# Kernel tuning notes

Hardware: AMD Instinct MI355X
Metric: run time of the kernel (lower is better)

## Reference

```python
import jax, jax.numpy as jnp
import numpy as np

B, T, C = 16, 512, 1024
D, K, W = 4096, 128, 8


def _scatter_topk(a, k, use_values):
    """Top-k along last axis; return dense array with top-k values (or 1.0) scattered, zeros elsewhere."""
    shp = a.shape
    a2 = a.reshape(-1, shp[-1])
    vals, idx = jax.lax.top_k(a2, k)
    rows = jnp.arange(a2.shape[0])[:, None]
    src = vals if use_values else jnp.ones_like(vals)
    return jnp.zeros_like(a2).at[rows, idx].set(src).reshape(shp)


def _window_topk(x, k, window_size):
    # x: (B, T, D)
    b, t, d = x.shape
    stride = max(1, window_size // 2)
    if stride >= t:
        num_windows, pad, t_pad = 1, 0, t
    else:
        num_windows = (t - window_size) // stride + 1
        required = (num_windows - 1) * stride + window_size
        pad = max(0, required - t)
        t_pad = t + pad
    if pad > 0:
        x = jnp.pad(x, ((0, 0), (0, pad), (0, 0)))
    starts = jnp.arange(num_windows) * stride                      # (NW,)
    tidx = starts[:, None] + jnp.arange(window_size)               # (NW, W)
    x_windows = x[:, tidx, :]                                      # (B, NW, W, D)
    window_sums = x_windows.sum(axis=2)                            # (B, NW, D)
    mask_windows = _scatter_topk(window_sums, k, use_values=False)  # (B, NW, D)
    votes = (x_windows * mask_windows[:, :, None, :]).reshape(b, num_windows * window_size, d)
    feature_votes = jnp.zeros((b, t_pad, d), x.dtype).at[:, tidx.reshape(-1)].add(votes)
    mask_combined = _scatter_topk(feature_votes, k, use_values=False)  # (B, Tp, D)
    x_sparse = x * mask_combined
    return x_sparse[:, :t - 0, :] if pad > 0 else x_sparse


def setup_inputs() -> dict:
    key = jax.random.key(0)
    ks = jax.random.split(key, 4)
    x_ssl = jax.random.normal(ks[0], (B, T, C), jnp.float32)
    W_dec = jax.random.normal(ks[1], (C, D), jnp.float32)
    W_dec = W_dec / jnp.linalg.norm(W_dec, axis=0, keepdims=True)
    W_enc = W_dec.T                                                # tied init, as in module
    W1 = jax.random.normal(ks[2], (256, D), jnp.float32) * (1.0 / np.sqrt(D))
    W2 = jax.random.normal(ks[3], (2, 256), jnp.float32) * (1.0 / np.sqrt(256))
    return dict(
        x_ssl=x_ssl, W_enc=W_enc, b_enc=jnp.zeros((D,), jnp.float32),
        W_dec=W_dec, b_dec=jnp.zeros((C,), jnp.float32),
        ln_g=jnp.ones((D,), jnp.float32), ln_b=jnp.zeros((D,), jnp.float32),
        W1=W1, b1=jnp.zeros((256,), jnp.float32),
        W2=W2, b2=jnp.zeros((2,), jnp.float32),
    )


def reference(x_ssl, W_enc, b_enc, W_dec, b_dec, ln_g, ln_b, W1, b1, W2, b2):
    b, t, c = x_ssl.shape
    x_flat = x_ssl.reshape(b * t, c)
    # SAE encode with window top-k (window_size=8 > 1 path)
    pre = jnp.einsum('nc,dc->nd', x_flat - b_dec, W_enc) + b_enc
    post_relu = jax.nn.relu(pre).reshape(b, t, -1)                 # (B, T, D)
    encoded = _window_topk(post_relu, K, W)                        # (B, T, D)
    encoded_flat = encoded.reshape(b * t, -1)
    # SAE decode + reconstruction loss
    x_recon = jnp.einsum('nd,cd->nc', encoded_flat, W_dec) + b_dec
    sae_loss = jnp.mean((x_recon - x_flat) ** 2)
    # classifier on pooled sparse features (dropout is inference no-op)
    pooled = encoded.mean(axis=1)                                  # (B, D) == AdaptiveAvgPool1d(1)
    mu = pooled.mean(axis=-1, keepdims=True)
    var = pooled.var(axis=-1, keepdims=True)
    ln = (pooled - mu) / jnp.sqrt(var + 1e-5) * ln_g + ln_b
    h = jax.nn.relu(ln @ W1.T + b1)
    logits = h @ W2.T + b2
    log_probs = jax.nn.log_softmax(logits, axis=-1)
    return log_probs, sae_loss
```

## Files before the change

### kernel.cpp

```cpp
#include <hip/hip_runtime.h>

#define BB   16
#define TT   512
#define CC   1024
#define DD   4096
#define NN   (BB*TT)
#define NWIN 127
#define KTOP 128

typedef __attribute__((ext_vector_type(8))) short short8;
typedef __attribute__((ext_vector_type(8))) unsigned short ushort8;
typedef _Float16 half8 __attribute__((ext_vector_type(8)));
typedef __attribute__((ext_vector_type(4))) float f32x4;

__device__ __forceinline__ unsigned short f2bf(float f) {
    unsigned u = __float_as_uint(f);
    unsigned r = (u + 0x7fffu + ((u >> 16) & 1u)) >> 16;
    return (unsigned short)r;
}
__device__ __forceinline__ unsigned short f2h(float f) {
    union { _Float16 h; unsigned short u; } c;
    c.h = (_Float16)f;
    return c.u;
}
__device__ __forceinline__ float h2f(unsigned short u) {
    union { unsigned short u; _Float16 h; } c;
    c.u = u;
    return (float)c.h;
}
__device__ __forceinline__ unsigned tokey(float f) {
    unsigned u = __float_as_uint(f);
    return (u & 0x80000000u) ? ~u : (u | 0x80000000u);
}
__device__ __forceinline__ void async_lds16(const void* g, void* l) {
    __builtin_amdgcn_global_load_lds((const __attribute__((address_space(1))) void*)g,
                                     (__attribute__((address_space(3))) void*)l, 16, 0, 0);
}

__device__ __forceinline__ unsigned wave_prefix_incl(unsigned v) {
    int lane = threadIdx.x & 63;
#pragma unroll
    for (int off = 1; off < 64; off <<= 1) {
        unsigned n = __shfl_up(v, off, 64);
        if (lane >= off) v += n;
    }
    return v;
}
__device__ __forceinline__ unsigned wave_suffix_incl(unsigned v) {
    int lane = threadIdx.x & 63;
#pragma unroll
    for (int off = 1; off < 64; off <<= 1) {
        unsigned n = __shfl_down(v, off, 64);
        if (lane + off < 64) v += n;
    }
    return v;
}

__device__ __forceinline__ unsigned select_top128(const unsigned* keys,
                                                  unsigned* hist, unsigned* shx) {
    const int tid = threadIdx.x, wid = tid >> 6, lane = tid & 63;
    const unsigned ZKEY = 0x80000000u;
    unsigned cpos = 0, cz = 0;
#pragma unroll
    for (int i = 0; i < 16; ++i) {
        cpos += (keys[i] > ZKEY);
        cz   += (keys[i] == ZKEY);
    }
    unsigned ppos = wave_prefix_incl(cpos);
    unsigned pz   = wave_prefix_incl(cz);
    if (lane == 63) { shx[wid] = ppos; shx[4 + wid] = pz; }
    __syncthreads();
    unsigned nz = shx[0] + shx[1] + shx[2] + shx[3];
    unsigned selbits = 0u;
    if (nz <= KTOP) {
        unsigned need = KTOP - nz;
        unsigned zr = pz - cz;
        if (wid > 0) zr += shx[4];
        if (wid > 1) zr += shx[5];
        if (wid > 2) zr += shx[6];
#pragma unroll
        for (int i = 0; i < 16; ++i) {
            bool sel = (keys[i] > ZKEY) || (keys[i] == ZKEY && zr < need);
            if (keys[i] == ZKEY) ++zr;
            selbits |= (sel ? 1u : 0u) << i;
        }
        return selbits;
    }
    unsigned k2[16];
#pragma unroll
    for (int i = 0; i < 16; ++i) k2[i] = (keys[i] > ZKEY) ? keys[i] : 0u;
    unsigned prefix = 0u, pmask = 0u, Kr = KTOP;
    for (int shift = 24; shift >= 0; shift -= 8) {
        hist[tid] = 0u; hist[256 + tid] = 0u; hist[512 + tid] = 0u; hist[768 + tid] = 0u;
        __syncthreads();
        unsigned* h = hist + (wid << 8);
#pragma unroll
        for (int i = 0; i < 16; ++i)
            if (k2[i] && (k2[i] & pmask) == prefix) atomicAdd(&h[(k2[i] >> shift) & 255u], 1u);
        __syncthreads();
        unsigned v = hist[tid] + hist[256 + tid] + hist[512 + tid] + hist[768 + tid];
        unsigned s = wave_suffix_incl(v);
        if (lane == 0) shx[wid] = s;
        __syncthreads();
        unsigned stot = s;
        if (wid == 0) stot += shx[1] + shx[2] + shx[3];
        else if (wid == 1) stot += shx[2] + shx[3];
        else if (wid == 2) stot += shx[3];
        unsigned above = stot - v;
        if (stot >= Kr && above < Kr) { shx[8] = (unsigned)tid; shx[9] = Kr - above; }
        __syncthreads();
        prefix |= shx[8] << shift;
        pmask |= 0xFFu << shift;
        Kr = shx[9];
    }
    unsigned T = prefix, need = Kr;
    unsigned ce = 0;
#pragma unroll
    for (int i = 0; i < 16; ++i) ce += (k2[i] == T);
    unsigned pe = wave_prefix_incl(ce);
    __syncthreads();
    if (lane == 63) shx[4 + wid] = pe;
    __syncthreads();
    unsigned er = pe - ce;
    if (wid > 0) er += shx[4];
    if (wid > 1) er += shx[5];
    if (wid > 2) er += shx[6];
#pragma unroll
    for (int i = 0; i < 16; ++i) {
        bool sel = (k2[i] > T) || (k2[i] == T && er < need);
        if (k2[i] == T) ++er;
        selbits |= (sel ? 1u : 0u) << i;
    }
    return selbits;
}

__global__ __launch_bounds__(256) void k_convert_all(const float* __restrict__ x,
                                                     const float* __restrict__ Wenc,
                                                     const float* __restrict__ Wdec,
                                                     const float* __restrict__ bdec,
                                                     unsigned short* __restrict__ xh,
                                                     unsigned short* __restrict__ wh,
                                                     unsigned short* __restrict__ wdh,
                                                     float* __restrict__ pooled_zero) {
    const int bid = blockIdx.x;
    if (bid < 8192) {
        size_t i = (size_t)bid * 256 + threadIdx.x;
        float4 v = ((const float4*)x)[i];
        size_t c = (i * 4) & (CC - 1);
        v.x -= bdec[c]; v.y -= bdec[c + 1]; v.z -= bdec[c + 2]; v.w -= bdec[c + 3];
        uint2 o;
        o.x = (unsigned)f2h(v.x) | ((unsigned)f2h(v.y) << 16);
        o.y = (unsigned)f2h(v.z) | ((unsigned)f2h(v.w) << 16);
        ((uint2*)xh)[i] = o;
    } else if (bid < 12288) {
        size_t i = (size_t)(bid - 8192) * 256 + threadIdx.x;
        float4 v = ((const float4*)Wenc)[i];
        uint2 o;
        o.x = (unsigned)f2h(v.x) | ((unsigned)f2h(v.y) << 16);
        o.y = (unsigned)f2h(v.z) | ((unsigned)f2h(v.w) << 16);
        ((uint2*)wh)[i] = o;
    } else if (bid < 16384) {
        size_t i = (size_t)(bid - 12288) * 256 + threadIdx.x;
        float4 v = ((const float4*)Wdec)[i];
        uint2 o;
        o.x = (unsigned)f2h(v.x) | ((unsigned)f2h(v.y) << 16);
        o.y = (unsigned)f2h(v.z) | ((unsigned)f2h(v.w) << 16);
        ((uint2*)wdh)[i] = o;
    } else {
        const int n4 = (BB * DD + 64) / 4;
        for (int i = threadIdx.x; i < n4; i += 256)
            ((float4*)pooled_zero)[i] = make_float4(0.f, 0.f, 0.f, 0.f);
    }
}

__device__ __forceinline__ void stage_tile_swz(const unsigned short* gbase, size_t ldk,
                                               unsigned short* lds, int wave, int lane) {
    const int sub = lane >> 3;
    const int cj  = (lane & 7) ^ sub;
#pragma unroll
    for (int i = 0; i < 4; ++i) {
        int n = wave * 4 + i;
        int r = n * 8 + sub;
        async_lds16(gbase + (size_t)r * ldk + cj * 8, lds + n * 512);
    }
}

__global__ __launch_bounds__(256) void k_gemm_enc_f16(const unsigned short* __restrict__ Ah,
                                                      const unsigned short* __restrict__ Bh,
                                                      const float* __restrict__ bias,
                                                      unsigned short* __restrict__ Cout,
                                                      float* __restrict__ gsum,
                                                      int Ndim, int Kdim) {
    __shared__ __align__(16) unsigned short smem[2 * 128 * 64];
    unsigned short* At = smem;
    unsigned short* Bt = smem + 128 * 64;
    float* cbuf = (float*)smem;
    const int tid = threadIdx.x, wave = tid >> 6, lane = tid & 63;
    unsigned nwg  = gridDim.x * gridDim.y;
    unsigned wid0 = blockIdx.y * gridDim.x + blockIdx.x;
    unsigned widx = (wid0 & 7u) * (nwg >> 3) + (wid0 >> 3);
    const int bn = (int)(widx % gridDim.x) * 128;
    const int bm = (int)(widx / gridDim.x) * 128;
    const int wm = (wave >> 1) * 64, wn = (wave & 1) * 64;
    const int rA = lane & 15, q8 = (lane >> 4) * 8, rp7 = rA & 7;
    const int q = lane >> 4, qr = q * 4, cl = lane & 15;
    f32x4 acc[4][4] = {};
    for (int k0 = 0; k0 < Kdim; k0 += 64) {
        __syncthreads();
        stage_tile_swz(Ah + (size_t)bm * Kdim + k0, Kdim, At, wave, lane);
        stage_tile_swz(Bh + (size_t)bn * Kdim + k0, Kdim, Bt, wave, lane);
        __syncthreads();
#pragma unroll
        for (int kk = 0; kk < 64; kk += 32) {
            const int sc = ((((kk + q8) >> 3) ^ rp7) << 3);
            half8 a[4], b[4];
#pragma unroll
            for (int mt = 0; mt < 4; ++mt) a[mt] = *(const half8*)(At + (wm + mt * 16 + rA) * 64 + sc);
#pragma unroll
            for (int nt = 0; nt < 4; ++nt) b[nt] = *(const half8*)(Bt + (wn + nt * 16 + rA) * 64 + sc);
#pragma unroll
            for (int mt = 0; mt < 4; ++mt)
#pragma unroll
                for (int nt = 0; nt < 4; ++nt)
                    acc[mt][nt] = __builtin_amdgcn_mfma_f32_16x16x32_f16(a[mt], b[nt], acc[mt][nt], 0, 0, 0);
        }
    }
    float bv[4];
#pragma unroll
    for (int nt = 0; nt < 4; ++nt) bv[nt] = bias[bn + wn + nt * 16 + cl];
#pragma unroll
    for (int p = 0; p < 2; ++p) {
        __syncthreads();
        if ((wave >> 1) == p) {
#pragma unroll
            for (int nt = 0; nt < 4; ++nt) {
                int lc = wn + nt * 16 + cl;
                int pcb = (lc >> 2) ^ (q << 1);
#pragma unroll
                for (int mt = 0; mt < 4; ++mt) {
#pragma unroll
                    for (int r = 0; r < 4; ++r) {
                        int lr = mt * 16 + qr + r;
                        float v = acc[mt][nt][r] + bv[nt];
                        v = v > 0.f ? v : 0.f;
                        cbuf[lr * 128 + pcb * 4 + (lc & 3)] = v;
                    }
                }
            }
        }
        __syncthreads();
#pragma unroll
        for (int i = 0; i < 2; ++i) {
            int gidx = i * 256 + tid;
            int grow = gidx >> 5;
            int colg = gidx & 31;
            float4 s = make_float4(0.f, 0.f, 0.f, 0.f);
#pragma unroll
            for (int j = 0; j < 4; ++j) {
                int lr = grow * 4 + j;
                int pcr = colg ^ (((lr >> 2) & 3) << 1);
                float4 v = *(const float4*)&cbuf[lr * 128 + pcr * 4];
                s.x += v.x; s.y += v.y; s.z += v.z; s.w += v.w;
                uint2 o;
                o.x = (unsigned)f2h(v.x) | ((unsigned)f2h(v.y) << 16);
                o.y = (unsigned)f2h(v.z) | ((unsigned)f2h(v.w) << 16);
                *(uint2*)&Cout[(size_t)(bm + p * 64 + lr) * Ndim + bn + colg * 4] = o;
            }
            if (gsum)
                *(float4*)&gsum[(size_t)((bm >> 2) + p * 16 + grow) * Ndim + bn + colg * 4] = s;
        }
    }
}

__global__ __launch_bounds__(256) void k_gemm_recon(const unsigned short* __restrict__ A,
                                                    size_t lda,
                                                    const unsigned short* __restrict__ Bm,
                                                    const float* __restrict__ bdec,
                                                    const float* __restrict__ X,
                                                    float* __restrict__ sae,
                                                    int Ndim, int Kdim) {
    __shared__ __align__(16) unsigned short At[2][128 * 64];
    __shared__ __align__(16) unsigned short Bt[2][128 * 64];
    __shared__ float red[256];
    const int tid = threadIdx.x, wave = tid >> 6, lane = tid & 63;
    unsigned nwg  = gridDim.x * gridDim.y;
    unsigned wid0 = blockIdx.y * gridDim.x + blockIdx.x;
    unsigned widx = (wid0 & 7u) * (nwg >> 3) + (wid0 >> 3);
    const int bn = (int)(widx % gridDim.x) * 128;
    const int bm = (int)(widx / gridDim.x) * 128;
    const int wm = (wave >> 1) * 64, wn = (wave & 1) * 64;
    const int rA = lane & 15, q8 = (lane >> 4) * 8, rp7 = rA & 7;
    f32x4 acc[4][4] = {};
    stage_tile_swz(A + (size_t)bm * lda, lda, At[0], wave, lane);
    stage_tile_swz(Bm + (size_t)bn * Kdim, Kdim, Bt[0], wave, lane);
    __syncthreads();
    for (int k0 = 0; k0 < Kdim; k0 += 64) {
        const int cur = (k0 >> 6) & 1;
        if (k0 + 64 < Kdim) {
            stage_tile_swz(A + (size_t)bm * lda + k0 + 64, lda, At[cur ^ 1], wave, lane);
            stage_tile_swz(Bm + (size_t)bn * Kdim + k0 + 64, Kdim, Bt[cur ^ 1], wave, lane);
        }
#pragma unroll
        for (int kk = 0; kk < 64; kk += 32) {
            const int sc = ((((kk + q8) >> 3) ^ rp7) << 3);
            half8 a[4], b[4];
#pragma unroll
            for (int mt = 0; mt < 4; ++mt) a[mt] = *(const half8*)(At[cur] + (wm + mt * 16 + rA) * 64 + sc);
#pragma unroll
            for (int nt = 0; nt < 4; ++nt) b[nt] = *(const half8*)(Bt[cur] + (wn + nt * 16 + rA) * 64 + sc);
#pragma unroll
            for (int mt = 0; mt < 4; ++mt)
#pragma unroll
                for (int nt = 0; nt < 4; ++nt)
                    acc[mt][nt] = __builtin_amdgcn_mfma_f32_16x16x32_f16(a[mt], b[nt], acc[mt][nt], 0, 0, 0);
        }
        __syncthreads();
    }
    const int cl = lane & 15, qr = (lane >> 4) * 4;
    float lsum = 0.f;
#pragma unroll
    for (int nt = 0; nt < 4; ++nt) {
        int col = bn + wn + nt * 16 + cl;
        float bv = bdec[col];
#pragma unroll
        for (int mt = 0; mt < 4; ++mt) {
            int row0 = bm + wm + mt * 16 + qr;
#pragma unroll
            for (int r = 0; r < 4; ++r) {
                float v = acc[mt][nt][r] + bv - X[(size_t)(row0 + r) * Ndim + col];
                lsum += v * v;
            }
        }
    }
    red[tid] = lsum;
    __syncthreads();
    for (int s = 128; s > 0; s >>= 1) { if (tid < s) red[tid] += red[tid + s]; __syncthreads(); }
    if (tid == 0) atomicAdd(sae, red[0]);
}

__global__ __launch_bounds__(256) void k_winsum_g(const float* __restrict__ gsum,
                                                  unsigned* __restrict__ wmask) {
    __shared__ unsigned hist[1024];
    __shared__ unsigned shx[16];
    __shared__ unsigned short halves[256];
    const int tid = threadIdx.x, w = blockIdx.x, b = blockIdx.y;
    const float* g0 = gsum + ((size_t)(b * 128 + w)) * DD + tid * 16;
    const float* g1 = g0 + DD;
    unsigned keys[16];
#pragma unroll
    for (int q = 0; q < 4; ++q) {
        float4 u = *(const float4*)(g0 + q * 4);
        float4 v = *(const float4*)(g1 + q * 4);
        keys[q * 4 + 0] = tokey(u.x + v.x);
        keys[q * 4 + 1] = tokey(u.y + v.y);
        keys[q * 4 + 2] = tokey(u.z + v.z);
        keys[q * 4 + 3] = tokey(u.w + v.w);
    }
    unsigned selbits = select_top128(keys, hist, shx);
    halves[tid] = (unsigned short)selbits;
    __syncthreads();
    if (tid < 128)
        wmask[(size_t)(b * NWIN + w) * 128 + tid] =
            (unsigned)halves[2 * tid] | ((unsigned)halves[2 * tid + 1] << 16);
}

__global__ __launch_bounds__(256) void k_winsum_p(const unsigned short* __restrict__ post,
                                                  unsigned* __restrict__ wmask) {
    __shared__ unsigned hist[1024];
    __shared__ unsigned shx[16];
    __shared__ unsigned short halves[256];
    const int tid = threadIdx.x, w = blockIdx.x, b = blockIdx.y;
    const unsigned short* base = post + (size_t)(b * TT + w * 4) * DD + tid * 16;
    float s[16] = {};
#pragma unroll
    for (int j = 0; j < 8; ++j) {
        const unsigned short* rp = base + (size_t)j * DD;
        ushort8 u0 = *(const ushort8*)rp;
        ushort8 u1 = *(const ushort8*)(rp + 8);
#pragma unroll
        for (int i = 0; i < 8; ++i) { s[i] += h2f(u0[i]); s[8 + i] += h2f(u1[i]); }
    }
    unsigned keys[16];
#pragma unroll
    for (int i = 0; i < 16; ++i) keys[i] = tokey(s[i]);
    unsigned selbits = select_top128(keys, hist, shx);
    halves[tid] = (unsigned short)selbits;
    __syncthreads();
    if (tid < 128)
        wmask[(size_t)(b * NWIN + w) * 128 + tid] =
            (unsigned)halves[2 * tid] | ((unsigned)halves[2 * tid + 1] << 16);
}

__global__ __launch_bounds__(256) void k_votes(unsigned short* __restrict__ post,
                                               const unsigned* __restrict__ wmask,
                                               float* __restrict__ pooled) {
    __shared__ unsigned long long cand[256];
    __shared__ unsigned char selbyte[DD];
    __shared__ unsigned shx[16];
    const int tid = threadIdx.x, wid = tid >> 6, lane = tid & 63;
    const int t = blockIdx.x, b = blockIdx.y;
    unsigned short* rp = post + (size_t)(b * TT + t) * DD;
    int w1 = t >> 2, w0 = w1 - 1;
    unsigned mw0 = 0u, mw1 = 0u;
    if (w0 >= 0)        mw0 = wmask[(size_t)(b * NWIN + w0) * 128 + (tid >> 1)];
    if (w1 <= NWIN - 1) mw1 = wmask[(size_t)(b * NWIN + w1) * 128 + (tid >> 1)];
    const int bbase = (tid & 1) * 16;
    const unsigned ZKEY = 0x80000000u;
    ushort8 raw0 = *(const ushort8*)(rp + tid * 16);
    ushort8 raw1 = *(const ushort8*)(rp + tid * 16 + 8);
    float vals[16];
#pragma unroll
    for (int i = 0; i < 8; ++i) { vals[i] = h2f(raw0[i]); vals[8 + i] = h2f(raw1[i]); }
    unsigned keys[16];
#pragma unroll
    for (int i = 0; i < 16; ++i) {
        float cov = (float)(((mw0 >> (bbase + i)) & 1u) + ((mw1 >> (bbase + i)) & 1u));
        keys[i] = tokey(vals[i] * cov);
    }
    unsigned cpos = 0, cz = 0;
#pragma unroll
    for (int i = 0; i < 16; ++i) {
        cpos += (keys[i] > ZKEY);
        cz   += (keys[i] == ZKEY);
    }
    unsigned ppos = wave_prefix_incl(cpos);
    unsigned pz   = wave_prefix_incl(cz);
    if (lane == 63) { shx[wid] = ppos; shx[4 + wid] = pz; }
    __syncthreads();
    unsigned nz = shx[0] + shx[1] + shx[2] + shx[3];
    unsigned selbits = 0u;
    if (nz <= KTOP) {
        unsigned need = KTOP - nz;
        unsigned zr = pz - cz;
        if (wid > 0) zr += shx[4];
        if (wid > 1) zr += shx[5];
        if (wid > 2) zr += shx[6];
#pragma unroll
        for (int i = 0; i < 16; ++i) {
            bool sel = (keys[i] > ZKEY) || (keys[i] == ZKEY && zr < need);
            if (keys[i] == ZKEY) ++zr;
            selbits |= (sel ? 1u : 0u) << i;
        }
    } else {
        *(uint4*)(selbyte + tid * 16) = make_uint4(0u, 0u, 0u, 0u);
        unsigned off = ppos - cpos;
        if (wid > 0) off += shx[0];
        if (wid > 1) off += shx[1];
        if (wid > 2) off += shx[2];
#pragma unroll
        for (int i = 0; i < 16; ++i) {
            if (keys[i] > ZKEY && off < 256u) {
                int d = tid * 16 + i;
                cand[off++] = ((unsigned long long)keys[i] << 12) | (unsigned)(4095 - d);
            }
        }
        __syncthreads();
        unsigned m = nz < 256u ? nz : 256u;
        if ((unsigned)tid < m) {
            unsigned long long mine = cand[tid];
            unsigned rank = 0;
            for (unsigned j = 0; j < m; ++j) rank += (cand[j] > mine);
            if (rank < KTOP) selbyte[4095 - (unsigned)(mine & 0xFFFu)] = 1;
        }
        __syncthreads();
#pragma unroll
        for (int i = 0; i < 16; ++i)
            selbits |= (selbyte[tid * 16 + i] ? 1u : 0u) << i;
    }
    ushort8 o0, o1;
#pragma unroll
    for (int i = 0; i < 8; ++i) {
        bool s0 = (selbits >> i) & 1u;
        bool s1 = (selbits >> (8 + i)) & 1u;
        o0[i] = s0 ? raw0[i] : (unsigned short)0;
        o1[i] = s1 ? raw1[i] : (unsigned short)0;
        if (s0 && vals[i] != 0.f)     atomicAdd(&pooled[(size_t)b * DD + tid * 16 + i], vals[i]);
        if (s1 && vals[8 + i] != 0.f) atomicAdd(&pooled[(size_t)b * DD + tid * 16 + 8 + i], vals[8 + i]);
    }
    *(ushort8*)(rp + tid * 16)     = o0;
    *(ushort8*)(rp + tid * 16 + 8) = o1;
}

__device__ __forceinline__ float block_sum(float v, float* red) {
    const int tid = threadIdx.x;
    red[tid] = v;
    __syncthreads();
    for (int s = 128; s > 0; s >>= 1) { if (tid < s) red[tid] += red[tid + s]; __syncthreads(); }
    float r = red[0];
    __syncthreads();
    return r;
}

__global__ __launch_bounds__(256) void k_head_ln(const float* __restrict__ pooled,
                                                 const float* __restrict__ lng,
                                                 const float* __restrict__ lnb,
                                                 float* __restrict__ lnout) {
    __shared__ float red[256];
    const int b = blockIdx.x, tid = threadIdx.x;
    float pv[16];
    float s = 0.f;
#pragma unroll
    for (int q = 0; q < 4; ++q) {
        float4 u = *(const float4*)(pooled + (size_t)b * DD + tid * 16 + q * 4);
        pv[q * 4 + 0] = u.x * (1.f / TT); pv[q * 4 + 1] = u.y * (1.f / TT);
        pv[q * 4 + 2] = u.z * (1.f / TT); pv[q * 4 + 3] = u.w * (1.f / TT);
        s += pv[q * 4 + 0] + pv[q * 4 + 1] + pv[q * 4 + 2] + pv[q * 4 + 3];
    }
    float mean = block_sum(s, red) * (1.f / (float)DD);
    float vs = 0.f;
#pragma unroll
    for (int i = 0; i < 16; ++i) { float c = pv[i] - mean; vs += c * c; }
    float var = block_sum(vs, red) * (1.f / (float)DD);
    float inv = rsqrtf(var + 1e-5f);
#pragma unroll
    for (int q = 0; q < 4; ++q) {
        float4 g = *(const float4*)(lng + tid * 16 + q * 4);
        float4 bb = *(const float4*)(lnb + tid * 16 + q * 4);
        float4 o;
        o.x = (pv[q * 4 + 0] - mean) * inv * g.x + bb.x;
        o.y = (pv[q * 4 + 1] - mean) * inv * g.y + bb.y;
        o.z = (pv[q * 4 + 2] - mean) * inv * g.z + bb.z;
        o.w = (pv[q * 4 + 3] - mean) * inv * g.w + bb.w;
        *(float4*)(lnout + (size_t)b * DD + tid * 16 + q * 4) = o;
    }
}

__global__ __launch_bounds__(256) void k_head_mlp(const float* __restrict__ lnout,
                                                  const float* __restrict__ W1,
                                                  const float* __restrict__ b1,
                                                  float* __restrict__ h) {
    const int gw = (blockIdx.x * 256 + threadIdx.x) >> 6;
    const int lane = threadIdx.x & 63;
    const int b = gw >> 8, row = gw & 255;
    const float* lp = lnout + (size_t)b * DD;
    const float* wr = W1 + (size_t)row * DD;
    float a = 0.f;
#pragma unroll
    for (int k = 0; k < DD / 64; ++k)
        a += lp[lane + 64 * k] * wr[lane + 64 * k];
#pragma unroll
    for (int off = 32; off > 0; off >>= 1) a += __shfl_down(a, off, 64);
    if (lane == 0) h[b * 256 + row] = fmaxf(a + b1[row], 0.f);
}

__global__ __launch_bounds__(256) void k_head_out(const float* __restrict__ h,
                                                  const float* __restrict__ W2,
                                                  const float* __restrict__ b2,
                                                  const float* __restrict__ sae,
                                                  float* __restrict__ out) {
    __shared__ float red[256];
    const int b = blockIdx.x, tid = threadIdx.x;
    float hv = h[b * 256 + tid];
    float l0 = block_sum(hv * W2[tid], red) + b2[0];
    float l1 = block_sum(hv * W2[256 + tid], red) + b2[1];
    if (tid == 0) {
        float m = fmaxf(l0, l1);
        float lse = m + logf(expf(l0 - m) + expf(l1 - m));
        out[2 * b] = l0 - lse;
        out[2 * b + 1] = l1 - lse;
        if (b == 0) out[32] = sae[0] * (1.f / (float)((size_t)NN * CC));
    }
}

extern "C" void kernel_launch(void* const* d_in, const int* in_sizes, int n_in,
                              void* d_out, int out_size, void* d_ws, size_t ws_size,
                              hipStream_t stream) {
    const float* x    = (const float*)d_in[0];
    const float* Wenc = (const float*)d_in[1];
    const float* benc = (const float*)d_in[2];
    const float* Wdec = (const float*)d_in[3];
    const float* bdec = (const float*)d_in[4];
    const float* lng  = (const float*)d_in[5];
    const float* lnb  = (const float*)d_in[6];
    const float* W1   = (const float*)d_in[7];
    const float* b1   = (const float*)d_in[8];
    const float* W2   = (const float*)d_in[9];
    const float* b2   = (const float*)d_in[10];
    float* out = (float*)d_out;

    char* ws = (char*)d_ws;
    unsigned short* post  = (unsigned short*)(ws + 0);
    unsigned short* xh16  = (unsigned short*)(ws + 67108864);
    unsigned short* scr   = (unsigned short*)(ws + 83886080);
    unsigned short* wh16  = (unsigned short*)(ws + 100663296);
    unsigned short* wd16  = (unsigned short*)(ws + 109051904);
    unsigned*       wmask = (unsigned*)(ws + 117440512);
    float*          pooled= (float*)(ws + 118480896);
    float*          sae   = (float*)(ws + 118743040);
    float*          gsum  = (float*)(ws + 118743296);
    const bool use_gsum = ws_size >= (size_t)118743296 + 33554432;
    float* gptr = use_gsum ? gsum : nullptr;
    float* lnout = (float*)xh16;
    float* hbuf  = (float*)scr;

    k_convert_all<<<dim3(16385), 256, 0, stream>>>(x, Wenc, Wdec, bdec, xh16, wh16, wd16, pooled);

    k_gemm_enc_f16<<<dim3(DD / 128, NN / 128), 256, 0, stream>>>(xh16, wh16, benc, post, gptr, DD, CC);
    if (use_gsum)
        k_winsum_g<<<dim3(NWIN, BB), 256, 0, stream>>>(gsum, wmask);
    else
        k_winsum_p<<<dim3(NWIN, BB), 256, 0, stream>>>(post, wmask);
    k_votes<<<dim3(TT, BB), 256, 0, stream>>>(post, wmask, pooled);
    k_gemm_recon<<<dim3(CC / 128, NN / 128), 256, 0, stream>>>(post, (size_t)DD,
                                                               wd16, bdec, x, sae, CC, DD);
    k_head_ln<<<dim3(BB), 256, 0, stream>>>(pooled, lng, lnb, lnout);
    k_head_mlp<<<dim3(1024), 256, 0, stream>>>(lnout, W1, b1, hbuf);
    k_head_out<<<dim3(BB), 256, 0, stream>>>(hbuf, W2, b2, sae, out);
}
```

Before: 442.2 us.

## Rewrite encoder and recon GEMMs with larger tiles and phased async pipeline

Both GEMMs are replaced: the encoder uses 256x256 tiles with 512 threads and the recon uses 256x128 tiles. Each streams K-slices through double-buffered LDS with global_load_lds, explicit vmcnt waits and barrier-delimited MFMA phases raised by s_setprio. The goal is to overlap global loads with MFMA work and raise arithmetic intensity per tile. In exchange it uses more LDS and registers, hardcodes the problem dimensions, and relies on hand-counted waitcnt values being correct.

Measured after the change: 440.3 us. About the same (-0.4%).

```diff
diff --git a/kernel.cpp b/kernel.cpp
--- a/kernel.cpp
+++ b/kernel.cpp
@@ -8,16 +8,10 @@
 #define NWIN 127
 #define KTOP 128
 
-typedef __attribute__((ext_vector_type(8))) short short8;
 typedef __attribute__((ext_vector_type(8))) unsigned short ushort8;
 typedef _Float16 half8 __attribute__((ext_vector_type(8)));
 typedef __attribute__((ext_vector_type(4))) float f32x4;
 
-__device__ __forceinline__ unsigned short f2bf(float f) {
-    unsigned u = __float_as_uint(f);
-    unsigned r = (u + 0x7fffu + ((u >> 16) & 1u)) >> 16;
-    return (unsigned short)r;
-}
 __device__ __forceinline__ unsigned short f2h(float f) {
     union { _Float16 h; unsigned short u; } c;
     c.h = (_Float16)f;
@@ -36,6 +30,12 @@
     __builtin_amdgcn_global_load_lds((const __attribute__((address_space(1))) void*)g,
                                      (__attribute__((address_space(3))) void*)l, 16, 0, 0);
 }
+
+#define PH_SYNC() do { __builtin_amdgcn_sched_barrier(0); __builtin_amdgcn_s_barrier(); \
+                       asm volatile("s_waitcnt lgkmcnt(0)" ::: "memory"); \
+                       __builtin_amdgcn_sched_barrier(0); __builtin_amdgcn_s_setprio(1); } while (0)
+#define PH_END()  do { __builtin_amdgcn_s_setprio(0); __builtin_amdgcn_sched_barrier(0); \
+                       __builtin_amdgcn_s_barrier(); } while (0)
 
 __device__ __forceinline__ unsigned wave_prefix_incl(unsigned v) {
     int lane = threadIdx.x & 63;
@@ -173,168 +173,268 @@
     }
 }
 
-__device__ __forceinline__ void stage_tile_swz(const unsigned short* gbase, size_t ldk,
-                                               unsigned short* lds, int wave, int lane) {
-    const int sub = lane >> 3;
-    const int cj  = (lane & 7) ^ sub;
-#pragma unroll
-    for (int i = 0; i < 4; ++i) {
-        int n = wave * 4 + i;
-        int r = n * 8 + sub;
-        async_lds16(gbase + (size_t)r * ldk + cj * 8, lds + n * 512);
-    }
-}
-
-__global__ __launch_bounds__(256) void k_gemm_enc_f16(const unsigned short* __restrict__ Ah,
-                                                      const unsigned short* __restrict__ Bh,
-                                                      const float* __restrict__ bias,
-                                                      unsigned short* __restrict__ Cout,
-                                                      float* __restrict__ gsum,
-                                                      int Ndim, int Kdim) {
-    __shared__ __align__(16) unsigned short smem[2 * 128 * 64];
-    unsigned short* At = smem;
-    unsigned short* Bt = smem + 128 * 64;
-    float* cbuf = (float*)smem;
-    const int tid = threadIdx.x, wave = tid >> 6, lane = tid & 63;
-    unsigned nwg  = gridDim.x * gridDim.y;
-    unsigned wid0 = blockIdx.y * gridDim.x + blockIdx.x;
-    unsigned widx = (wid0 & 7u) * (nwg >> 3) + (wid0 >> 3);
-    const int bn = (int)(widx % gridDim.x) * 128;
-    const int bm = (int)(widx / gridDim.x) * 128;
-    const int wm = (wave >> 1) * 64, wn = (wave & 1) * 64;
-    const int rA = lane & 15, q8 = (lane >> 4) * 8, rp7 = rA & 7;
-    const int q = lane >> 4, qr = q * 4, cl = lane & 15;
-    f32x4 acc[4][4] = {};
-    for (int k0 = 0; k0 < Kdim; k0 += 64) {
-        __syncthreads();
-        stage_tile_swz(Ah + (size_t)bm * Kdim + k0, Kdim, At, wave, lane);
-        stage_tile_swz(Bh + (size_t)bn * Kdim + k0, Kdim, Bt, wave, lane);
-        __syncthreads();
-#pragma unroll
-        for (int kk = 0; kk < 64; kk += 32) {
-            const int sc = ((((kk + q8) >> 3) ^ rp7) << 3);
-            half8 a[4], b[4];
-#pragma unroll
-            for (int mt = 0; mt < 4; ++mt) a[mt] = *(const half8*)(At + (wm + mt * 16 + rA) * 64 + sc);
-#pragma unroll
-            for (int nt = 0; nt < 4; ++nt) b[nt] = *(const half8*)(Bt + (wn + nt * 16 + rA) * 64 + sc);
-#pragma unroll
-            for (int mt = 0; mt < 4; ++mt)
-#pragma unroll
-                for (int nt = 0; nt < 4; ++nt)
-                    acc[mt][nt] = __builtin_amdgcn_mfma_f32_16x16x32_f16(a[mt], b[nt], acc[mt][nt], 0, 0, 0);
-        }
-    }
+__global__ __launch_bounds__(512, 2) void k_gemm_enc_256(const unsigned short* __restrict__ Ah,
+                                                         const unsigned short* __restrict__ Bh,
+                                                         const float* __restrict__ bias,
+                                                         unsigned short* __restrict__ Cout,
+                                                         float* __restrict__ gsum) {
+    __shared__ __align__(16) unsigned short lds[2][4][128 * 64];
+    const int tid = threadIdx.x, w = tid >> 6, lane = tid & 63;
+    const int bm = blockIdx.y * 256, bn = blockIdx.x * 256;
+    const int wr = w >> 2, wc = w & 3;
+    const int rA = lane & 15, q = lane >> 4;
+    const int sc0 = (q ^ (rA & 7)) << 3, sc1 = ((4 + q) ^ (rA & 7)) << 3;
+    const int s_rt = w * 16 + (lane >> 3);
+    const int s_ct = ((lane & 7) ^ (lane >> 3)) * 8;
+    const unsigned short* Abase = Ah + ((size_t)(bm + s_rt)) * 1024 + s_ct;
+    const unsigned short* Bbase = Bh + ((size_t)(bn + s_rt)) * 1024 + s_ct;
+
+    auto STAGE = [&](const unsigned short* gb, int rowoff, int kt, unsigned short* reg) {
+        const unsigned short* g = gb + (size_t)rowoff * 1024 + (kt << 6);
+        async_lds16(g, reg + w * 1024);
+        async_lds16(g + 8 * 1024, reg + w * 1024 + 512);
+    };
+
+    half8 a[4][2], b[4][2];
+    f32x4 acc[8][4] = {};
+
+    auto RDA4 = [&](const unsigned short* reg) {
+#pragma unroll
+        for (int mf = 0; mf < 4; ++mf) {
+            const unsigned short* p = reg + (wr * 64 + mf * 16 + rA) * 64;
+            a[mf][0] = *(const half8*)(p + sc0);
+            a[mf][1] = *(const half8*)(p + sc1);
+        }
+    };
+    auto RDB2 = [&](const unsigned short* reg, int nb) {
+#pragma unroll
+        for (int nf = 0; nf < 2; ++nf) {
+            const unsigned short* p = reg + (wc * 32 + nf * 16 + rA) * 64;
+            b[nb + nf][0] = *(const half8*)(p + sc0);
+            b[nb + nf][1] = *(const half8*)(p + sc1);
+        }
+    };
+    auto MF = [&](int mb, int nb) {
+#pragma unroll
+        for (int kk = 0; kk < 2; ++kk)
+#pragma unroll
+            for (int mf = 0; mf < 4; ++mf)
+#pragma unroll
+                for (int nf = 0; nf < 2; ++nf)
+                    acc[mb + mf][nb + nf] = __builtin_amdgcn_mfma_f32_16x16x32_f16(
+                        a[mf][kk], b[nb + nf][kk], acc[mb + mf][nb + nf], 0, 0, 0);
+    };
+
+    STAGE(Abase,   0, 0, lds[0][0]);
+    STAGE(Bbase,   0, 0, lds[0][2]);
+    STAGE(Abase, 128, 0, lds[0][1]);
+    STAGE(Bbase, 128, 0, lds[0][3]);
+    STAGE(Abase,   0, 1, lds[1][0]);
+    STAGE(Bbase,   0, 1, lds[1][2]);
+    STAGE(Abase, 128, 1, lds[1][1]);
+    asm volatile("s_waitcnt vmcnt(6)" ::: "memory");
+    __builtin_amdgcn_s_barrier();
+
+    for (int i = 0; i < 8; ++i) {
+        const int ko  = (2 * i + 1) & 15;
+        const int ke  = (2 * i + 2) & 15;
+        const int ko2 = (2 * i + 3) & 15;
+        RDA4(lds[0][0]); RDB2(lds[0][2], 0);
+        STAGE(Bbase, 128, ko, lds[1][3]);
+        PH_SYNC(); MF(0, 0); PH_END();
+        RDB2(lds[0][3], 2);
+        STAGE(Abase, 0, ke, lds[0][0]);
+        PH_SYNC(); MF(0, 2); PH_END();
+        RDA4(lds[0][1]);
+        STAGE(Bbase, 0, ke, lds[0][2]);
+        PH_SYNC(); MF(4, 0); PH_END();
+        STAGE(Abase, 128, ke, lds[0][1]);
+        asm volatile("s_waitcnt vmcnt(6)" ::: "memory");
+        PH_SYNC(); MF(4, 2); PH_END();
+        RDA4(lds[1][0]); RDB2(lds[1][2], 0);
+        STAGE(Bbase, 128, ke, lds[0][3]);
+        PH_SYNC(); MF(0, 0); PH_END();
+        RDB2(lds[1][3], 2);
+        STAGE(Abase, 0, ko2, lds[1][0]);
+        PH_SYNC(); MF(0, 2); PH_END();
+        RDA4(lds[1][1]);
+        STAGE(Bbase, 0, ko2, lds[1][2]);
+        PH_SYNC(); MF(4, 0); PH_END();
+        STAGE(Abase, 128, ko2, lds[1][1]);
+        asm volatile("s_waitcnt vmcnt(6)" ::: "memory");
+        PH_SYNC(); MF(4, 2); PH_END();
+    }
+
+    asm volatile("s_waitcnt vmcnt(0)" ::: "memory");
+    __syncthreads();
+    float* cbuf = (float*)&lds[0][0][0];
+    const int cl = rA, qr = q * 4;
     float bv[4];
 #pragma unroll
-    for (int nt = 0; nt < 4; ++nt) bv[nt] = bias[bn + wn + nt * 16 + cl];
+    for (int nf = 0; nf < 4; ++nf)
+        bv[nf] = bias[bn + ((nf < 2) ? wc * 32 + nf * 16 : 128 + wc * 32 + (nf - 2) * 16) + cl];
+    const int rg = tid >> 4, seg = tid & 15;
 #pragma unroll
     for (int p = 0; p < 2; ++p) {
-        __syncthreads();
-        if ((wave >> 1) == p) {
-#pragma unroll
-            for (int nt = 0; nt < 4; ++nt) {
-                int lc = wn + nt * 16 + cl;
-                int pcb = (lc >> 2) ^ (q << 1);
-#pragma unroll
-                for (int mt = 0; mt < 4; ++mt) {
-#pragma unroll
-                    for (int r = 0; r < 4; ++r) {
-                        int lr = mt * 16 + qr + r;
-                        float v = acc[mt][nt][r] + bv[nt];
-                        v = v > 0.f ? v : 0.f;
-                        cbuf[lr * 128 + pcb * 4 + (lc & 3)] = v;
-                    }
+        if (p) __syncthreads();
+#pragma unroll
+        for (int mf = 0; mf < 4; ++mf) {
+            int lrow0 = wr * 64 + mf * 16 + qr;
+#pragma unroll
+            for (int nf = 0; nf < 4; ++nf) {
+                int col = ((nf < 2) ? wc * 32 + nf * 16 : 128 + wc * 32 + (nf - 2) * 16) + cl;
+#pragma unroll
+                for (int r = 0; r < 4; ++r) {
+                    int lrow = lrow0 + r;
+                    float v = acc[p * 4 + mf][nf][r] + bv[nf];
+                    v = v > 0.f ? v : 0.f;
+                    cbuf[lrow * 256 + (col ^ (((lrow >> 2) & 7) << 2))] = v;
                 }
             }
         }
         __syncthreads();
-#pragma unroll
-        for (int i = 0; i < 2; ++i) {
-            int gidx = i * 256 + tid;
-            int grow = gidx >> 5;
-            int colg = gidx & 31;
-            float4 s = make_float4(0.f, 0.f, 0.f, 0.f);
-#pragma unroll
-            for (int j = 0; j < 4; ++j) {
-                int lr = grow * 4 + j;
-                int pcr = colg ^ (((lr >> 2) & 3) << 1);
-                float4 v = *(const float4*)&cbuf[lr * 128 + pcr * 4];
-                s.x += v.x; s.y += v.y; s.z += v.z; s.w += v.w;
-                uint2 o;
-                o.x = (unsigned)f2h(v.x) | ((unsigned)f2h(v.y) << 16);
-                o.y = (unsigned)f2h(v.z) | ((unsigned)f2h(v.w) << 16);
-                *(uint2*)&Cout[(size_t)(bm + p * 64 + lr) * Ndim + bn + colg * 4] = o;
-            }
-            if (gsum)
-                *(float4*)&gsum[(size_t)((bm >> 2) + p * 16 + grow) * Ndim + bn + colg * 4] = s;
-        }
-    }
-}
-
-__global__ __launch_bounds__(256) void k_gemm_recon(const unsigned short* __restrict__ A,
-                                                    size_t lda,
-                                                    const unsigned short* __restrict__ Bm,
-                                                    const float* __restrict__ bdec,
-                                                    const float* __restrict__ X,
-                                                    float* __restrict__ sae,
-                                                    int Ndim, int Kdim) {
-    __shared__ __align__(16) unsigned short At[2][128 * 64];
-    __shared__ __align__(16) unsigned short Bt[2][128 * 64];
-    __shared__ float red[256];
-    const int tid = threadIdx.x, wave = tid >> 6, lane = tid & 63;
-    unsigned nwg  = gridDim.x * gridDim.y;
-    unsigned wid0 = blockIdx.y * gridDim.x + blockIdx.x;
-    unsigned widx = (wid0 & 7u) * (nwg >> 3) + (wid0 >> 3);
-    const int bn = (int)(widx % gridDim.x) * 128;
-    const int bm = (int)(widx / gridDim.x) * 128;
-    const int wm = (wave >> 1) * 64, wn = (wave & 1) * 64;
-    const int rA = lane & 15, q8 = (lane >> 4) * 8, rp7 = rA & 7;
+        f32x4 gs0 = {}, gs1 = {}, gs2 = {}, gs3 = {};
+#pragma unroll
+        for (int i2 = 0; i2 < 4; ++i2) {
+            const int lrow = rg * 4 + i2;
+            const f32x4* crow = (const f32x4*)cbuf + lrow * 64;
+            f32x4 v0 = crow[(seg * 4 + 0) ^ (rg & 7)];
+            f32x4 v1 = crow[(seg * 4 + 1) ^ (rg & 7)];
+            f32x4 v2 = crow[(seg * 4 + 2) ^ (rg & 7)];
+            f32x4 v3 = crow[(seg * 4 + 3) ^ (rg & 7)];
+            uint4 o0, o1;
+            o0.x = (unsigned)f2h(v0[0]) | ((unsigned)f2h(v0[1]) << 16);
+            o0.y = (unsigned)f2h(v0[2]) | ((unsigned)f2h(v0[3]) << 16);
+            o0.z = (unsigned)f2h(v1[0]) | ((unsigned)f2h(v1[1]) << 16);
+            o0.w = (unsigned)f2h(v1[2]) | ((unsigned)f2h(v1[3]) << 16);
+            o1.x = (unsigned)f2h(v2[0]) | ((unsigned)f2h(v2[1]) << 16);
+            o1.y = (unsigned)f2h(v2[2]) | ((unsigned)f2h(v2[3]) << 16);
+            o1.z = (unsigned)f2h(v3[0]) | ((unsigned)f2h(v3[1]) << 16);
+            o1.w = (unsigned)f2h(v3[2]) | ((unsigned)f2h(v3[3]) << 16);
+            size_t gr = (size_t)(bm + p * 128 + lrow) * 4096 + bn + seg * 16;
+            *(uint4*)&Cout[gr] = o0;
+            *(uint4*)&Cout[gr + 8] = o1;
+            gs0 += v0; gs1 += v1; gs2 += v2; gs3 += v3;
+        }
+        if (gsum) {
+            size_t gr = ((size_t)(bm >> 2) + p * 32 + rg) * 4096 + bn + seg * 16;
+            *(f32x4*)&gsum[gr + 0]  = gs0;
+            *(f32x4*)&gsum[gr + 4]  = gs1;
+            *(f32x4*)&gsum[gr + 8]  = gs2;
+            *(f32x4*)&gsum[gr + 12] = gs3;
+        }
+    }
+}
+
+__global__ __launch_bounds__(512, 2) void k_gemm_recon_256(const unsigned short* __restrict__ Ap,
+                                                           const unsigned short* __restrict__ Bp,
+                                                           const float* __restrict__ bdec,
+                                                           const float* __restrict__ X,
+                                                           float* __restrict__ sae) {
+    __shared__ __align__(16) unsigned short lds[2][3][128 * 64];
+    __shared__ float red[512];
+    const int tid = threadIdx.x, w = tid >> 6, lane = tid & 63;
+    const int bm = blockIdx.y * 256, bn = blockIdx.x * 128;
+    const int wr = w >> 1, wc = w & 1;
+    const int rA = lane & 15, q = lane >> 4;
+    const int sc0 = (q ^ (rA & 7)) << 3, sc1 = ((4 + q) ^ (rA & 7)) << 3;
+    const int s_rt = w * 16 + (lane >> 3);
+    const int s_ct = ((lane & 7) ^ (lane >> 3)) * 8;
+    const unsigned short* Abase = Ap + ((size_t)(bm + s_rt)) * 4096 + s_ct;
+    const unsigned short* Bbase = Bp + ((size_t)(bn + s_rt)) * 4096 + s_ct;
+
+    auto STAGE = [&](const unsigned short* gb, int rowoff, int kt, unsigned short* reg) {
+        const unsigned short* g = gb + (size_t)rowoff * 4096 + (kt << 6);
+        async_lds16(g, reg + w * 1024);
+        async_lds16(g + 8 * 4096, reg + w * 1024 + 512);
+    };
+
+    half8 a[2][2], b[4][2];
     f32x4 acc[4][4] = {};
-    stage_tile_swz(A + (size_t)bm * lda, lda, At[0], wave, lane);
-    stage_tile_swz(Bm + (size_t)bn * Kdim, Kdim, Bt[0], wave, lane);
-    __syncthreads();
-    for (int k0 = 0; k0 < Kdim; k0 += 64) {
-        const int cur = (k0 >> 6) & 1;
-        if (k0 + 64 < Kdim) {
-            stage_tile_swz(A + (size_t)bm * lda + k0 + 64, lda, At[cur ^ 1], wave, lane);
-            stage_tile_swz(Bm + (size_t)bn * Kdim + k0 + 64, Kdim, Bt[cur ^ 1], wave, lane);
-        }
-#pragma unroll
-        for (int kk = 0; kk < 64; kk += 32) {
-            const int sc = ((((kk + q8) >> 3) ^ rp7) << 3);
-            half8 a[4], b[4];
-#pragma unroll
-            for (int mt = 0; mt < 4; ++mt) a[mt] = *(const half8*)(At[cur] + (wm + mt * 16 + rA) * 64 + sc);
-#pragma unroll
-            for (int nt = 0; nt < 4; ++nt) b[nt] = *(const half8*)(Bt[cur] + (wn + nt * 16 + rA) * 64 + sc);
-#pragma unroll
-            for (int mt = 0; mt < 4; ++mt)
-#pragma unroll
-                for (int nt = 0; nt < 4; ++nt)
-                    acc[mt][nt] = __builtin_amdgcn_mfma_f32_16x16x32_f16(a[mt], b[nt], acc[mt][nt], 0, 0, 0);
-        }
-        __syncthreads();
-    }
-    const int cl = lane & 15, qr = (lane >> 4) * 4;
+
+    auto RDA2 = [&](const unsigned short* reg) {
+#pragma unroll
+        for (int mf = 0; mf < 2; ++mf) {
+            const unsigned short* p = reg + (wr * 32 + mf * 16 + rA) * 64;
+            a[mf][0] = *(const half8*)(p + sc0);
+            a[mf][1] = *(const half8*)(p + sc1);
+        }
+    };
+    auto RDB2 = [&](const unsigned short* reg, int nb) {
+#pragma unroll
+        for (int nf = 0; nf < 2; ++nf) {
+            const unsigned short* p = reg + ((nb ? 64 : 0) + wc * 32 + nf * 16 + rA) * 64;
+            b[nb + nf][0] = *(const half8*)(p + sc0);
+            b[nb + nf][1] = *(const half8*)(p + sc1);
+        }
+    };
+    auto MF = [&](int mb, int nb) {
+#pragma unroll
+        for (int kk = 0; kk < 2; ++kk)
+#pragma unroll
+            for (int mf = 0; mf < 2; ++mf)
+#pragma unroll
+                for (int nf = 0; nf < 2; ++nf)
+                    acc[mb + mf][nb + nf] = __builtin_amdgcn_mfma_f32_16x16x32_f16(
+                        a[mf][kk], b[nb + nf][kk], acc[mb + mf][nb + nf], 0, 0, 0);
+    };
+
+    STAGE(Abase,   0, 0, lds[0][0]);
+    STAGE(Bbase,   0, 0, lds[0][2]);
+    STAGE(Abase, 128, 0, lds[0][1]);
+    STAGE(Abase,   0, 1, lds[1][0]);
+    STAGE(Bbase,   0, 1, lds[1][2]);
+    asm volatile("s_waitcnt vmcnt(4)" ::: "memory");
+    __builtin_amdgcn_s_barrier();
+
+    for (int i = 0; i < 32; ++i) {
+        const int ko  = (2 * i + 1) & 63;
+        const int ke  = (2 * i + 2) & 63;
+        const int ko2 = (2 * i + 3) & 63;
+        RDA2(lds[0][0]); RDB2(lds[0][2], 0);
+        STAGE(Abase, 128, ko, lds[1][1]);
+        PH_SYNC(); MF(0, 0); PH_END();
+        RDB2(lds[0][2], 2);
+        STAGE(Abase, 0, ke, lds[0][0]);
+        PH_SYNC(); MF(0, 2); PH_END();
+        RDA2(lds[0][1]);
+        STAGE(Bbase, 0, ke, lds[0][2]);
+        PH_SYNC(); MF(2, 0); PH_END();
+        asm volatile("s_waitcnt vmcnt(4)" ::: "memory");
+        PH_SYNC(); MF(2, 2); PH_END();
+        RDA2(lds[1][0]); RDB2(lds[1][2], 0);
+        STAGE(Abase, 128, ke, lds[0][1]);
+        PH_SYNC(); MF(0, 0); PH_END();
+        RDB2(lds[1][2], 2);
+        STAGE(Abase, 0, ko2, lds[1][0]);
+        PH_SYNC(); MF(0, 2); PH_END();
+        RDA2(lds[1][1]);
+        STAGE(Bbase, 0, ko2, lds[1][2]);
+        PH_SYNC(); MF(2, 0); PH_END();
+        asm volatile("s_waitcnt vmcnt(4)" ::: "memory");
+        PH_SYNC(); MF(2, 2); PH_END();
+    }
+
+    asm volatile("s_waitcnt vmcnt(0)" ::: "memory");
+    const int cl = rA, qr = q * 4;
     float lsum = 0.f;
 #pragma unroll
-    for (int nt = 0; nt < 4; ++nt) {
-        int col = bn + wn + nt * 16 + cl;
-        float bv = bdec[col];
-#pragma unroll
-        for (int mt = 0; mt < 4; ++mt) {
-            int row0 = bm + wm + mt * 16 + qr;
+    for (int mf = 0; mf < 4; ++mf) {
+        int row0 = bm + ((mf < 2) ? wr * 32 + mf * 16 : 128 + wr * 32 + (mf - 2) * 16) + qr;
+#pragma unroll
+        for (int nf = 0; nf < 4; ++nf) {
+            int col = bn + ((nf < 2) ? wc * 32 + nf * 16 : 64 + wc * 32 + (nf - 2) * 16) + cl;
+            float bvv = bdec[col];
 #pragma unroll
             for (int r = 0; r < 4; ++r) {
-                float v = acc[mt][nt][r] + bv - X[(size_t)(row0 + r) * Ndim + col];
+                float v = acc[mf][nf][r] + bvv - X[(size_t)(row0 + r) * 1024 + col];
                 lsum += v * v;
             }
         }
     }
     red[tid] = lsum;
     __syncthreads();
-    for (int s = 128; s > 0; s >>= 1) { if (tid < s) red[tid] += red[tid + s]; __syncthreads(); }
+    for (int s = 256; s > 0; s >>= 1) { if (tid < s) red[tid] += red[tid + s]; __syncthreads(); }
     if (tid == 0) atomicAdd(sae, red[0]);
 }
 
@@ -595,14 +695,13 @@
 
     k_convert_all<<<dim3(16385), 256, 0, stream>>>(x, Wenc, Wdec, bdec, xh16, wh16, wd16, pooled);
 
-    k_gemm_enc_f16<<<dim3(DD / 128, NN / 128), 256, 0, stream>>>(xh16, wh16, benc, post, gptr, DD, CC);
+    k_gemm_enc_256<<<dim3(DD / 256, NN / 256), 512, 0, stream>>>(xh16, wh16, benc, post, gptr);
     if (use_gsum)
         k_winsum_g<<<dim3(NWIN, BB), 256, 0, stream>>>(gsum, wmask);
     else
         k_winsum_p<<<dim3(NWIN, BB), 256, 0, stream>>>(post, wmask);
     k_votes<<<dim3(TT, BB), 256, 0, stream>>>(post, wmask, pooled);
-    k_gemm_recon<<<dim3(CC / 128, NN / 128), 256, 0, stream>>>(post, (size_t)DD,
-                                                               wd16, bdec, x, sae, CC, DD);
+    k_gemm_recon_256<<<dim3(CC / 128, NN / 256), 512, 0, stream>>>(post, wd16, bdec, x, sae);
     k_head_ln<<<dim3(BB), 256, 0, stream>>>(pooled, lng, lnb, lnout);
     k_head_mlp<<<dim3(1024), 256, 0, stream>>>(lnout, W1, b1, hbuf);
     k_head_out<<<dim3(BB), 256, 0, stream>>>(hbuf, W2, b2, sae, out);
```
